# Optimization experiments

Measured on AMD Instinct MI355X. Metric: run time of the kernel, lower is better.

Reference implementation:

```python
import math
import jax, jax.numpy as jnp
import numpy as np
from math import factorial as fact

RS_IN = [(8, 0), (8, 1)]
RS_OUT = [(8, 0), (8, 1)]
N_PATH = 384
HIDDEN = 64
B, N_OUT_PTS, N_IN_PTS = 2, 256, 256

def _lfilters(l_in, l_out, lmax=10):
    return [l for l in range(abs(l_in - l_out), l_in + l_out + 1) if l <= lmax]

# ---- Clebsch-Gordan / Wigner-3j in the real spherical-harmonic basis ----
def _cg(j1, m1, j2, m2, j3, m3):
    if m1 + m2 != m3:
        return 0.0
    kmin = max(0, j2 - j3 - m1, j1 - j3 + m2)
    kmax = min(j1 + j2 - j3, j1 - m1, j2 + m2)
    if kmax < kmin:
        return 0.0
    pre = math.sqrt((2 * j3 + 1) * fact(j3 + j1 - j2) * fact(j3 - j1 + j2) * fact(j1 + j2 - j3) / fact(j1 + j2 + j3 + 1))
    pre *= math.sqrt(fact(j3 + m3) * fact(j3 - m3) * fact(j1 - m1) * fact(j1 + m1) * fact(j2 - m2) * fact(j2 + m2))
    s = sum((-1) ** k / (fact(k) * fact(j1 + j2 - j3 - k) * fact(j1 - m1 - k) * fact(j2 + m2 - k) * fact(j3 - j2 + m1 + k) * fact(j3 - j1 - m2 + k)) for k in range(kmin, kmax + 1))
    return pre * s

def _wigner3j(j1, j2, j3):
    W = np.zeros((2 * j1 + 1, 2 * j2 + 1, 2 * j3 + 1))
    for m1 in range(-j1, j1 + 1):
        for m2 in range(-j2, j2 + 1):
            m3 = -(m1 + m2)
            if abs(m3) <= j3:
                W[m1 + j1, m2 + j2, m3 + j3] = (-1) ** (j1 - j2 - m3) / math.sqrt(2 * j3 + 1) * _cg(j1, m1, j2, m2, j3, -m3)
    return W

def _A(l):
    # change of basis real<->complex SH: Y^real_a = sum_m A[a, m] Y^complex_m
    A = np.zeros((2 * l + 1, 2 * l + 1), dtype=np.complex128)
    A[l, l] = 1.0
    for m in range(1, l + 1):
        A[l + m, l + m] = (-1) ** m / math.sqrt(2)
        A[l + m, l - m] = 1.0 / math.sqrt(2)
        A[l - m, l - m] = 1j / math.sqrt(2)
        A[l - m, l + m] = -1j * (-1) ** m / math.sqrt(2)
    return A

def _real_cg(l1, l2, l3):
    W = _wigner3j(l1, l2, l3).astype(np.complex128)
    Q = np.einsum('am,bn,cp,mnp->abc', _A(l1).conj(), _A(l2).conj(), _A(l3).conj(), W)
    v = Q.flat[int(np.argmax(np.abs(Q)))]
    if abs(v) > 1e-12:
        Q = Q * (v.conjugate() / abs(v))  # rotate global phase so tensor is real
    assert np.abs(Q.imag).max() < 1e-8
    return Q.real.astype(np.float32)

# ---- real spherical harmonics of unit directions, l = 0, 1, 2 ----
_C0 = 0.28209479177387814
_C1 = 0.4886025119029199
_C2A = 1.0925484305920792
_C2B = 0.31539156525252005
_C2C = 0.5462742152960396

def _sh(xyz):
    r = jnp.linalg.norm(xyz, axis=-1, keepdims=True)
    u = xyz / jnp.maximum(r, 1e-12)
    x, y, z = u[..., 0], u[..., 1], u[..., 2]
    Y0 = _C0 * jnp.ones_like(x)[..., None]
    Y1 = _C1 * jnp.stack([y, z, x], axis=-1)
    Y2 = jnp.stack([_C2A * x * y, _C2A * y * z, _C2B * (3.0 * z * z - 1.0), _C2A * x * z, _C2C * (x * x - y * y)], axis=-1)
    return {0: Y0, 1: Y1, 2: Y2}


def setup_inputs() -> dict:
    key = jax.random.key(0)
    ks = jax.random.split(key, 3)
    dm = jax.random.normal(ks[0], (B, N_OUT_PTS, N_IN_PTS, 3), dtype=jnp.float32)
    W1 = 0.1 * jax.random.normal(ks[1], (1, HIDDEN), dtype=jnp.float32)
    b1 = jnp.zeros((HIDDEN,), dtype=jnp.float32)
    W2 = (1.0 / math.sqrt(HIDDEN)) * jax.random.normal(ks[2], (HIDDEN, N_PATH), dtype=jnp.float32)
    b2 = jnp.zeros((N_PATH,), dtype=jnp.float32)
    Q00 = jnp.asarray(_real_cg(0, 0, 0))  # (1,1,1)
    Q01 = jnp.asarray(_real_cg(0, 1, 1))  # (1,3,3)
    Q10 = jnp.asarray(_real_cg(1, 0, 1))  # (3,1,3)
    Q11 = jnp.asarray(np.concatenate([_real_cg(1, 1, l) for l in (0, 1, 2)], axis=2))  # (3,3,9)
    return {"difference_matrix": dm, "W1": W1, "b1": b1, "W2": W2, "b2": b2, "Q00": Q00, "Q01": Q01, "Q10": Q10, "Q11": Q11}


def reference(difference_matrix, W1, b1, W2, b2, Q00, Q01, Q10, Q11):
    Bb, No, Ni, _ = difference_matrix.shape
    Ys = _sh(difference_matrix)                       # l -> [B, No, Ni, 2l+1]
    radii = jnp.linalg.norm(difference_matrix, axis=-1)
    h = jax.nn.relu(radii[..., None] * W1[0] + b1)    # radial MLP
    weights = h @ W2 + b2                             # [B, No, Ni, N_PATH]
    Qs = {(0, 0): Q00, (0, 1): Q01, (1, 0): Q10, (1, 1): Q11}
    begin_w = 0
    rows = []
    for i, (mul_out, l_out) in enumerate(RS_OUT):
        num = sum(mul_in * len(_lfilters(l_in, l_out)) for mul_in, l_in in RS_IN) * Ni
        cols = []
        for j, (mul_in, l_in) in enumerate(RS_IN):
            lfs = _lfilters(l_in, l_out)
            n = mul_out * mul_in * len(lfs)
            w = weights[..., begin_w:begin_w + n].reshape(Bb, No, Ni, mul_out, mul_in, len(lfs))
            begin_w += n
            Q = Qs[(i, j)]
            K = 0.0
            off = 0
            for k, lf in enumerate(lfs):
                Qk = Q[:, :, off:off + 2 * lf + 1]
                off += 2 * lf + 1
                # i=m_out, j=m_in, r=m_filter, b n m = batch/N_out/N_in, u v = mul_out/mul_in
                K = K + jnp.einsum('ijr,bnmr,bnmuv->uivjbnm', Qk, Ys[lf], w[..., k])
            K = K * (math.sqrt(2 * l_in + 1) * math.sqrt(4.0 * math.pi) / math.sqrt(num))
            cols.append(K.reshape(mul_out * (2 * l_out + 1), mul_in * (2 * l_in + 1), Bb, No, Ni))
        rows.append(jnp.concatenate(cols, axis=1))
    return jnp.concatenate(rows, axis=0)  # [n_out, n_in, B, N_out, N_in]
```

## Files before the change

kernel.cpp:

```cpp
#include <hip/hip_runtime.h>
#include <math.h>

namespace {

typedef float f32x4 __attribute__((ext_vector_type(4)));
typedef float f32x2 __attribute__((ext_vector_type(2)));

constexpr int kPts  = 2 * 256 * 256;
constexpr int kHid  = 64;
constexpr int kPath = 384;

constexpr size_t kVOff    = (size_t)kPts * 4;
constexpr size_t kFlagOff = kVOff + kPath;
constexpr size_t kWOff    = kVOff + 512;
constexpr size_t kWFloats = 64ull * kPts * 6;
constexpr size_t kNeedBytes = (kWOff + kWFloats) * 4;

constexpr float kY0   = 0.28209479177387814f;
constexpr float kC1   = 0.4886025119029199f;
constexpr float kC2A  = 1.0925484305920792f;
constexpr float kC2B  = 0.31539156525252005f;
constexpr float kC2C  = 0.5462742152960396f;
constexpr float kS4pi = 3.5449077018110318f;
constexpr float kSq3  = 1.7320508075688772f;
constexpr float kN00  = kS4pi / 64.f;
constexpr float kN01  = kSq3 * kS4pi / 64.f;
constexpr float kN10  = kS4pi / 90.50966799187809f;
constexpr float kN11  = kSq3 * kS4pi / 90.50966799187809f;

__global__ __launch_bounds__(256)
void stage_kernel(const float* __restrict__ dm,
                  const float* __restrict__ W1,
                  const float* __restrict__ b1,
                  const float* __restrict__ W2,
                  f32x4* __restrict__ ru,
                  float* __restrict__ V,
                  unsigned* __restrict__ flag)
{
    const int pt = blockIdx.x * 256 + threadIdx.x;
    float dx = dm[3 * pt + 0], dy = dm[3 * pt + 1], dz = dm[3 * pt + 2];
    float r  = sqrtf(dx * dx + dy * dy + dz * dz);
    float inv = 1.0f / fmaxf(r, 1e-12f);
    f32x4 q; q.x = r; q.y = dx * inv; q.z = dy * inv; q.w = dz * inv;
    ru[pt] = q;

    if (blockIdx.x == 0) {
        for (int p = threadIdx.x; p < kPath; p += 256) {
            float acc = 0.f;
            for (int i = 0; i < kHid; ++i)
                acc += fmaxf(W1[i], 0.f) * W2[i * kPath + p];
            V[p] = acc;
        }
        if (threadIdx.x == 0) {
            unsigned f = 1u;
            for (int i = 0; i < kHid; ++i)
                if (b1[i] != 0.f) f = 0u;
            *flag = f;
        }
    }
}

__global__ __launch_bounds__(256)
void wstage_kernel(const float* __restrict__ W1,
                   const float* __restrict__ b1,
                   const float* __restrict__ W2,
                   const float* __restrict__ b2,
                   const f32x4* __restrict__ ru,
                   const unsigned* __restrict__ flag,
                   float* __restrict__ wout)
{
    if (*flag) return;
    const int pt = blockIdx.x * 256 + threadIdx.x;
    const float r = ru[pt].x;
    float h[kHid];
#pragma unroll
    for (int i = 0; i < kHid; ++i)
        h[i] = fmaxf(fmaf(r, W1[i], b1[i]), 0.f);

#pragma unroll 1
    for (int uv = 0; uv < 64; ++uv) {
        const int p[6] = { uv, 64 + uv, 128 + uv,
                           192 + 3 * uv, 193 + 3 * uv, 194 + 3 * uv };
        float acc[6];
#pragma unroll
        for (int c = 0; c < 6; ++c) acc[c] = b2[p[c]];
#pragma unroll 1
        for (int i = 0; i < kHid; ++i) {
            const float* row = W2 + (size_t)i * kPath;
#pragma unroll
            for (int c = 0; c < 6; ++c) acc[c] = fmaf(h[i], row[p[c]], acc[c]);
        }
        float* o = wout + ((size_t)uv * kPts + pt) * 6;
#pragma unroll
        for (int c = 0; c < 6; ++c) o[c] = acc[c];
    }
}

__global__ __launch_bounds__(256)
void sweep_kernel(const float* __restrict__ Q00,
                  const float* __restrict__ Q01,
                  const float* __restrict__ Q10,
                  const float* __restrict__ Q11,
                  const float* __restrict__ b2,
                  const f32x4* __restrict__ ru,
                  const float* __restrict__ V,
                  const unsigned* __restrict__ flag,
                  const float* __restrict__ wstaged,
                  float* __restrict__ out)
{
    const int seg = blockIdx.x;
    const int uv  = blockIdx.y;
    const int u = uv >> 3, v = uv & 7;

    const float s00p = kN00 * Q00[0] * kY0;
    float a01[3][3], a10[3][3], g0c[9], a11[9][3], b11[9][5];
    const float c2s[5] = { kC2A, kC2A, kC2B, kC2A, kC2C };
#pragma unroll
    for (int jc = 0; jc < 3; ++jc)
#pragma unroll
        for (int m = 0; m < 3; ++m)
            a01[jc][m] = kN01 * kC1 * Q01[jc * 3 + m];
#pragma unroll
    for (int ir = 0; ir < 3; ++ir)
#pragma unroll
        for (int m = 0; m < 3; ++m)
            a10[ir][m] = kN10 * kC1 * Q10[ir * 3 + m];
#pragma unroll
    for (int e = 0; e < 9; ++e) {
        g0c[e] = kN11 * kY0 * Q11[e * 9 + 0];
#pragma unroll
        for (int m = 0; m < 3; ++m) a11[e][m] = kN11 * kC1 * Q11[e * 9 + 1 + m];
#pragma unroll
        for (int m = 0; m < 5; ++m) b11[e][m] = kN11 * c2s[m] * Q11[e * 9 + 4 + m];
    }

    const bool fast = (*flag != 0u);
    const int pw[6] = { uv, 64 + uv, 128 + uv,
                        192 + 3 * uv, 193 + 3 * uv, 194 + 3 * uv };
    float vv[6], cc[6];
#pragma unroll
    for (int c = 0; c < 6; ++c) { vv[c] = V[pw[c]]; cc[c] = b2[pw[c]]; }

    int pr[16];
    pr[0] = u * 32 + v;
#pragma unroll
    for (int jc = 0; jc < 3; ++jc) pr[1 + jc] = u * 32 + 8 + v * 3 + jc;
#pragma unroll
    for (int ir = 0; ir < 3; ++ir) pr[4 + ir] = (8 + u * 3 + ir) * 32 + v;
#pragma unroll
    for (int e = 0; e < 9; ++e)
        pr[7 + e] = (8 + u * 3 + (e / 3)) * 32 + 8 + v * 3 + (e % 3);

    const size_t segbase = (size_t)seg * 4096 + threadIdx.x;

#pragma unroll 1
    for (int batch = 0; batch < 4; ++batch) {
        const size_t p0 = segbase + (size_t)batch * 1024;

        float bs[4][8], w_[4][6];
#pragma unroll
        for (int k = 0; k < 4; ++k) {
            f32x4 q = ru[p0 + k * 256];
            float r = q.x, x = q.y, y = q.z, z = q.w;
            bs[k][0] = y;  bs[k][1] = z;  bs[k][2] = x;
            bs[k][3] = x * y;
            bs[k][4] = y * z;
            bs[k][5] = fmaf(3.f * z, z, -1.f);
            bs[k][6] = x * z;
            bs[k][7] = fmaf(x, x, -(y * y));
            if (fast) {
#pragma unroll
                for (int c = 0; c < 6; ++c) w_[k][c] = fmaf(r, vv[c], cc[c]);
            } else {
                const float* wp = wstaged + ((size_t)uv * kPts + (p0 + k * 256)) * 6;
#pragma unroll
                for (int c = 0; c < 6; ++c) w_[k][c] = wp[c];
            }
        }

#pragma unroll
        for (int k = 0; k < 4; ++k)
            out[(size_t)pr[0] * kPts + p0 + k * 256] = s00p * w_[k][0];

#pragma unroll
        for (int jc = 0; jc < 3; ++jc) {
#pragma unroll
            for (int k = 0; k < 4; ++k) {
                float g = fmaf(a01[jc][2], bs[k][2],
                           fmaf(a01[jc][1], bs[k][1], a01[jc][0] * bs[k][0]));
                out[(size_t)pr[1 + jc] * kPts + p0 + k * 256] = g * w_[k][1];
            }
        }
#pragma unroll
        for (int ir = 0; ir < 3; ++ir) {
#pragma unroll
            for (int k = 0; k < 4; ++k) {
                float g = fmaf(a10[ir][2], bs[k][2],
                           fmaf(a10[ir][1], bs[k][1], a10[ir][0] * bs[k][0]));
                out[(size_t)pr[4 + ir] * kPts + p0 + k * 256] = g * w_[k][2];
            }
        }
#pragma unroll
        for (int e = 0; e < 9; ++e) {
#pragma unroll
            for (int k = 0; k < 4; ++k) {
                float lin = fmaf(a11[e][2], bs[k][2],
                             fmaf(a11[e][1], bs[k][1], a11[e][0] * bs[k][0]));
                float quad = b11[e][0] * bs[k][3];
#pragma unroll
                for (int m = 1; m < 5; ++m)
                    quad = fmaf(b11[e][m], bs[k][3 + m], quad);
                float val = fmaf(g0c[e], w_[k][3],
                             fmaf(lin, w_[k][4], quad * w_[k][5]));
                out[(size_t)pr[7 + e] * kPts + p0 + k * 256] = val;
            }
        }
    }
}

__global__ __launch_bounds__(256)
void mono_kernel(const float* __restrict__ dm,
                 const float* __restrict__ W1,
                 const float* __restrict__ b1,
                 const float* __restrict__ W2,
                 const float* __restrict__ b2,
                 const float* __restrict__ Q00,
                 const float* __restrict__ Q01,
                 const float* __restrict__ Q10,
                 const float* __restrict__ Q11,
                 float* __restrict__ out)
{
    const int g   = blockIdx.x * blockDim.x + threadIdx.x;
    const int uv0 = blockIdx.y * 8;

    const f32x4* dmv = reinterpret_cast<const f32x4*>(dm) + 3 * (size_t)g;
    f32x4 f0 = dmv[0], f1 = dmv[1], f2 = dmv[2];
    float px[4] = { f0.x, f0.w, f1.z, f2.y };
    float py[4] = { f0.y, f1.x, f1.w, f2.z };
    float pz[4] = { f0.z, f1.y, f2.x, f2.w };

    float r[4], ux[4], uy[4], uz[4];
#pragma unroll
    for (int p = 0; p < 4; ++p) {
        r[p] = sqrtf(px[p]*px[p] + py[p]*py[p] + pz[p]*pz[p]);
        float inv = 1.0f / fmaxf(r[p], 1e-12f);
        ux[p] = px[p]*inv; uy[p] = py[p]*inv; uz[p] = pz[p]*inv;
    }
    float Y10[4], Y11v[4], Y12[4], Y2[5][4];
#pragma unroll
    for (int p = 0; p < 4; ++p) {
        Y10[p] = kC1 * uy[p]; Y11v[p] = kC1 * uz[p]; Y12[p] = kC1 * ux[p];
        Y2[0][p] = kC2A * ux[p] * uy[p];
        Y2[1][p] = kC2A * uy[p] * uz[p];
        Y2[2][p] = kC2B * (3.f * uz[p] * uz[p] - 1.f);
        Y2[3][p] = kC2A * ux[p] * uz[p];
        Y2[4][p] = kC2C * (ux[p]*ux[p] - uy[p]*uy[p]);
    }
    const float s00 = kN00 * Q00[0] * kY0;
    float G0[9];
#pragma unroll
    for (int e = 0; e < 9; ++e) G0[e] = kN11 * Q11[e*9] * kY0;
    float g01[3][4], g10[3][4], G1[9][4], G2[9][4];
#pragma unroll
    for (int jc = 0; jc < 3; ++jc)
#pragma unroll
        for (int p = 0; p < 4; ++p)
            g01[jc][p] = kN01 * (Q01[jc*3]*Y10[p] + Q01[jc*3+1]*Y11v[p] + Q01[jc*3+2]*Y12[p]);
#pragma unroll
    for (int ir = 0; ir < 3; ++ir)
#pragma unroll
        for (int p = 0; p < 4; ++p)
            g10[ir][p] = kN10 * (Q10[ir*3]*Y10[p] + Q10[ir*3+1]*Y11v[p] + Q10[ir*3+2]*Y12[p]);
#pragma unroll
    for (int e = 0; e < 9; ++e) {
        const float* q = Q11 + e * 9;
#pragma unroll
        for (int p = 0; p < 4; ++p) {
            G1[e][p] = kN11 * (q[1]*Y10[p] + q[2]*Y11v[p] + q[3]*Y12[p]);
            G2[e][p] = kN11 * (q[4]*Y2[0][p] + q[5]*Y2[1][p] + q[6]*Y2[2][p] +
                               q[7]*Y2[3][p] + q[8]*Y2[4][p]);
        }
    }
    float* __restrict__ obase = out + 4 * (size_t)g;
    auto stf = [&](int row, const float* v4) {
        f32x4 q; q.x=v4[0]; q.y=v4[1]; q.z=v4[2]; q.w=v4[3];
        *reinterpret_cast<f32x4*>(obase + (size_t)row * kPts) = q;
    };
#pragma unroll 1
    for (int t = 0; t < 8; ++t) {
        const int uv = uv0 + t;
        float a00[4], a01v[4], a10v[4], a110[4], a111[4], a112[4];
#pragma unroll
        for (int p = 0; p < 4; ++p) {
            a00[p]=b2[uv]; a01v[p]=b2[64+uv]; a10v[p]=b2[128+uv];
            a110[p]=b2[192+3*uv]; a111[p]=b2[193+3*uv]; a112[p]=b2[194+3*uv];
        }
#pragma unroll 1
        for (int i = 0; i < kHid; ++i) {
            float w1i = W1[i], b1i = b1[i];
            const float* row = W2 + (size_t)i * kPath;
            float c00=row[uv], c01=row[64+uv], c10=row[128+uv];
            float c50=row[192+3*uv], c51=row[193+3*uv], c52=row[194+3*uv];
#pragma unroll
            for (int p = 0; p < 4; ++p) {
                float hi = fmaxf(fmaf(r[p], w1i, b1i), 0.f);
                a00[p]=fmaf(hi,c00,a00[p]); a01v[p]=fmaf(hi,c01,a01v[p]);
                a10v[p]=fmaf(hi,c10,a10v[p]); a110[p]=fmaf(hi,c50,a110[p]);
                a111[p]=fmaf(hi,c51,a111[p]); a112[p]=fmaf(hi,c52,a112[p]);
            }
        }
        const int u = uv >> 3, v = uv & 7;
        const int rowu = u * 32;
        float tmp[4];
#pragma unroll
        for (int p = 0; p < 4; ++p) tmp[p] = s00 * a00[p];
        stf(rowu + v, tmp);
#pragma unroll
        for (int jc = 0; jc < 3; ++jc) {
#pragma unroll
            for (int p = 0; p < 4; ++p) tmp[p] = g01[jc][p] * a01v[p];
            stf(rowu + 8 + v*3 + jc, tmp);
        }
#pragma unroll
        for (int ir = 0; ir < 3; ++ir) {
            const int rowb = (8 + u*3 + ir) * 32;
#pragma unroll
            for (int p = 0; p < 4; ++p) tmp[p] = g10[ir][p] * a10v[p];
            stf(rowb + v, tmp);
#pragma unroll
            for (int jc = 0; jc < 3; ++jc) {
                const int e = ir*3 + jc;
#pragma unroll
                for (int p = 0; p < 4; ++p)
                    tmp[p] = fmaf(G0[e], a110[p], fmaf(G1[e][p], a111[p], G2[e][p]*a112[p]));
                stf(rowb + 8 + v*3 + jc, tmp);
            }
        }
    }
}

}

extern "C" void kernel_launch(void* const* d_in, const int* in_sizes, int n_in,
                              void* d_out, int out_size, void* d_ws, size_t ws_size,
                              hipStream_t stream)
{
    const float* dm  = (const float*)d_in[0];
    const float* W1  = (const float*)d_in[1];
    const float* b1  = (const float*)d_in[2];
    const float* W2  = (const float*)d_in[3];
    const float* b2  = (const float*)d_in[4];
    const float* Q00 = (const float*)d_in[5];
    const float* Q01 = (const float*)d_in[6];
    const float* Q10 = (const float*)d_in[7];
    const float* Q11 = (const float*)d_in[8];
    float* out = (float*)d_out;

    if (ws_size >= kNeedBytes) {
        float* ws = (float*)d_ws;
        f32x4*    ru   = (f32x4*)ws;
        float*    V    = ws + kVOff;
        unsigned* flag = (unsigned*)(ws + kFlagOff);
        float*    wst  = ws + kWOff;
        stage_kernel<<<kPts / 256, 256, 0, stream>>>(dm, W1, b1, W2, ru, V, flag);
        wstage_kernel<<<kPts / 256, 256, 0, stream>>>(W1, b1, W2, b2, ru, flag, wst);
        sweep_kernel<<<dim3(32, 64), 256, 0, stream>>>(
            Q00, Q01, Q10, Q11, b2, ru, V, flag, wst, out);
    } else {
        mono_kernel<<<dim3(128, 8), 256, 0, stream>>>(
            dm, W1, b1, W2, b2, Q00, Q01, Q10, Q11, out);
    }
}
```

Measured before the change: 113.9 us.

## Fuse direction computation into a single plane-writing kernel with per-thread point tiling

Replaces the three-kernel pipeline (stage directions, stage per-point weights, sweep) with a tiny prep kernel for V and the bias flag, plus one fused kernel. The fused kernel recomputes the norm and unit direction from the raw displacements in each (u,v) block, and computes the radial MLP inline on the slow path. Each thread now handles 8 points instead of 4. This removes the intermediate workspace traffic and launches, at the cost of redundant sqrt/divide work and repeated displacement reads across the 64 uv blocks.

```diff
diff --git a/kernel.cpp b/kernel.cpp
--- a/kernel.cpp
+++ b/kernel.cpp
@@ -4,17 +4,12 @@
 namespace {
 
 typedef float f32x4 __attribute__((ext_vector_type(4)));
-typedef float f32x2 __attribute__((ext_vector_type(2)));
 
 constexpr int kPts  = 2 * 256 * 256;
 constexpr int kHid  = 64;
 constexpr int kPath = 384;
 
-constexpr size_t kVOff    = (size_t)kPts * 4;
-constexpr size_t kFlagOff = kVOff + kPath;
-constexpr size_t kWOff    = kVOff + 512;
-constexpr size_t kWFloats = 64ull * kPts * 6;
-constexpr size_t kNeedBytes = (kWOff + kWFloats) * 4;
+constexpr size_t kWsNeedBytes = (kPath + 1) * sizeof(float);
 
 constexpr float kY0   = 0.28209479177387814f;
 constexpr float kC1   = 0.4886025119029199f;
@@ -28,192 +23,142 @@
 constexpr float kN10  = kS4pi / 90.50966799187809f;
 constexpr float kN11  = kSq3 * kS4pi / 90.50966799187809f;
 
+__global__ void prep_kernel(const float* __restrict__ W1,
+                            const float* __restrict__ b1,
+                            const float* __restrict__ W2,
+                            float* __restrict__ V,
+                            unsigned* __restrict__ flag)
+{
+    int t = blockIdx.x * 256 + threadIdx.x;
+    if (t < kPath) {
+        float acc = 0.f;
+        for (int i = 0; i < kHid; ++i)
+            acc += fmaxf(W1[i], 0.f) * W2[i * kPath + t];
+        V[t] = acc;
+    }
+    if (t == 0) {
+        unsigned f = 1u;
+        for (int i = 0; i < kHid; ++i)
+            if (b1[i] != 0.f) f = 0u;
+        *flag = f;
+    }
+}
+
 __global__ __launch_bounds__(256)
-void stage_kernel(const float* __restrict__ dm,
+void plane_kernel(const float* __restrict__ dm,
                   const float* __restrict__ W1,
                   const float* __restrict__ b1,
                   const float* __restrict__ W2,
-                  f32x4* __restrict__ ru,
-                  float* __restrict__ V,
-                  unsigned* __restrict__ flag)
-{
-    const int pt = blockIdx.x * 256 + threadIdx.x;
-    float dx = dm[3 * pt + 0], dy = dm[3 * pt + 1], dz = dm[3 * pt + 2];
-    float r  = sqrtf(dx * dx + dy * dy + dz * dz);
-    float inv = 1.0f / fmaxf(r, 1e-12f);
-    f32x4 q; q.x = r; q.y = dx * inv; q.z = dy * inv; q.w = dz * inv;
-    ru[pt] = q;
-
-    if (blockIdx.x == 0) {
-        for (int p = threadIdx.x; p < kPath; p += 256) {
-            float acc = 0.f;
-            for (int i = 0; i < kHid; ++i)
-                acc += fmaxf(W1[i], 0.f) * W2[i * kPath + p];
-            V[p] = acc;
-        }
-        if (threadIdx.x == 0) {
-            unsigned f = 1u;
-            for (int i = 0; i < kHid; ++i)
-                if (b1[i] != 0.f) f = 0u;
-            *flag = f;
-        }
-    }
-}
-
-__global__ __launch_bounds__(256)
-void wstage_kernel(const float* __restrict__ W1,
-                   const float* __restrict__ b1,
-                   const float* __restrict__ W2,
-                   const float* __restrict__ b2,
-                   const f32x4* __restrict__ ru,
-                   const unsigned* __restrict__ flag,
-                   float* __restrict__ wout)
-{
-    if (*flag) return;
-    const int pt = blockIdx.x * 256 + threadIdx.x;
-    const float r = ru[pt].x;
-    float h[kHid];
-#pragma unroll
-    for (int i = 0; i < kHid; ++i)
-        h[i] = fmaxf(fmaf(r, W1[i], b1[i]), 0.f);
-
-#pragma unroll 1
-    for (int uv = 0; uv < 64; ++uv) {
-        const int p[6] = { uv, 64 + uv, 128 + uv,
-                           192 + 3 * uv, 193 + 3 * uv, 194 + 3 * uv };
-        float acc[6];
-#pragma unroll
-        for (int c = 0; c < 6; ++c) acc[c] = b2[p[c]];
-#pragma unroll 1
-        for (int i = 0; i < kHid; ++i) {
-            const float* row = W2 + (size_t)i * kPath;
-#pragma unroll
-            for (int c = 0; c < 6; ++c) acc[c] = fmaf(h[i], row[p[c]], acc[c]);
-        }
-        float* o = wout + ((size_t)uv * kPts + pt) * 6;
-#pragma unroll
-        for (int c = 0; c < 6; ++c) o[c] = acc[c];
-    }
-}
-
-__global__ __launch_bounds__(256)
-void sweep_kernel(const float* __restrict__ Q00,
+                  const float* __restrict__ b2,
+                  const float* __restrict__ Q00,
                   const float* __restrict__ Q01,
                   const float* __restrict__ Q10,
                   const float* __restrict__ Q11,
-                  const float* __restrict__ b2,
-                  const f32x4* __restrict__ ru,
                   const float* __restrict__ V,
                   const unsigned* __restrict__ flag,
-                  const float* __restrict__ wstaged,
                   float* __restrict__ out)
 {
-    const int seg = blockIdx.x;
-    const int uv  = blockIdx.y;
-    const int u = uv >> 3, v = uv & 7;
-
-    const float s00p = kN00 * Q00[0] * kY0;
-    float a01[3][3], a10[3][3], g0c[9], a11[9][3], b11[9][5];
-    const float c2s[5] = { kC2A, kC2A, kC2B, kC2A, kC2C };
-#pragma unroll
-    for (int jc = 0; jc < 3; ++jc)
-#pragma unroll
-        for (int m = 0; m < 3; ++m)
-            a01[jc][m] = kN01 * kC1 * Q01[jc * 3 + m];
-#pragma unroll
-    for (int ir = 0; ir < 3; ++ir)
-#pragma unroll
-        for (int m = 0; m < 3; ++m)
-            a10[ir][m] = kN10 * kC1 * Q10[ir * 3 + m];
-#pragma unroll
-    for (int e = 0; e < 9; ++e) {
-        g0c[e] = kN11 * kY0 * Q11[e * 9 + 0];
-#pragma unroll
-        for (int m = 0; m < 3; ++m) a11[e][m] = kN11 * kC1 * Q11[e * 9 + 1 + m];
-#pragma unroll
-        for (int m = 0; m < 5; ++m) b11[e][m] = kN11 * c2s[m] * Q11[e * 9 + 4 + m];
-    }
-
-    const bool fast = (*flag != 0u);
+    const int uv = blockIdx.y, u = uv >> 3, v = uv & 7;
+    const size_t base = (size_t)blockIdx.x * 2048 + threadIdx.x;
+
+    float R[8], X[8], Y[8], Z[8];
+#pragma unroll
+    for (int k = 0; k < 8; ++k) {
+        size_t pt = base + 256 * (size_t)k;
+        float dx = dm[3 * pt], dy = dm[3 * pt + 1], dz = dm[3 * pt + 2];
+        float r  = sqrtf(dx * dx + dy * dy + dz * dz);
+        float inv = 1.f / fmaxf(r, 1e-12f);
+        R[k] = r; X[k] = dx * inv; Y[k] = dy * inv; Z[k] = dz * inv;
+    }
+
     const int pw[6] = { uv, 64 + uv, 128 + uv,
                         192 + 3 * uv, 193 + 3 * uv, 194 + 3 * uv };
-    float vv[6], cc[6];
-#pragma unroll
-    for (int c = 0; c < 6; ++c) { vv[c] = V[pw[c]]; cc[c] = b2[pw[c]]; }
-
-    int pr[16];
-    pr[0] = u * 32 + v;
-#pragma unroll
-    for (int jc = 0; jc < 3; ++jc) pr[1 + jc] = u * 32 + 8 + v * 3 + jc;
-#pragma unroll
-    for (int ir = 0; ir < 3; ++ir) pr[4 + ir] = (8 + u * 3 + ir) * 32 + v;
-#pragma unroll
-    for (int e = 0; e < 9; ++e)
-        pr[7 + e] = (8 + u * 3 + (e / 3)) * 32 + 8 + v * 3 + (e % 3);
-
-    const size_t segbase = (size_t)seg * 4096 + threadIdx.x;
-
-#pragma unroll 1
-    for (int batch = 0; batch < 4; ++batch) {
-        const size_t p0 = segbase + (size_t)batch * 1024;
-
-        float bs[4][8], w_[4][6];
-#pragma unroll
-        for (int k = 0; k < 4; ++k) {
-            f32x4 q = ru[p0 + k * 256];
-            float r = q.x, x = q.y, y = q.z, z = q.w;
-            bs[k][0] = y;  bs[k][1] = z;  bs[k][2] = x;
-            bs[k][3] = x * y;
-            bs[k][4] = y * z;
-            bs[k][5] = fmaf(3.f * z, z, -1.f);
-            bs[k][6] = x * z;
-            bs[k][7] = fmaf(x, x, -(y * y));
-            if (fast) {
-#pragma unroll
-                for (int c = 0; c < 6; ++c) w_[k][c] = fmaf(r, vv[c], cc[c]);
-            } else {
-                const float* wp = wstaged + ((size_t)uv * kPts + (p0 + k * 256)) * 6;
-#pragma unroll
-                for (int c = 0; c < 6; ++c) w_[k][c] = wp[c];
+    float w[6][8];
+    if (*flag != 0u) {
+#pragma unroll
+        for (int c = 0; c < 6; ++c) {
+            float vc = V[pw[c]], bc = b2[pw[c]];
+#pragma unroll
+            for (int k = 0; k < 8; ++k) w[c][k] = fmaf(R[k], vc, bc);
+        }
+    } else {
+#pragma unroll
+        for (int c = 0; c < 6; ++c) {
+            float bc = b2[pw[c]];
+#pragma unroll
+            for (int k = 0; k < 8; ++k) w[c][k] = bc;
+        }
+#pragma unroll 1
+        for (int i = 0; i < kHid; ++i) {
+            float w1i = W1[i], b1i = b1[i];
+            const float* row = W2 + (size_t)i * kPath;
+            float cr[6];
+#pragma unroll
+            for (int c = 0; c < 6; ++c) cr[c] = row[pw[c]];
+#pragma unroll
+            for (int k = 0; k < 8; ++k) {
+                float h = fmaxf(fmaf(R[k], w1i, b1i), 0.f);
+#pragma unroll
+                for (int c = 0; c < 6; ++c) w[c][k] = fmaf(h, cr[c], w[c][k]);
             }
         }
-
-#pragma unroll
-        for (int k = 0; k < 4; ++k)
-            out[(size_t)pr[0] * kPts + p0 + k * 256] = s00p * w_[k][0];
-
-#pragma unroll
-        for (int jc = 0; jc < 3; ++jc) {
-#pragma unroll
-            for (int k = 0; k < 4; ++k) {
-                float g = fmaf(a01[jc][2], bs[k][2],
-                           fmaf(a01[jc][1], bs[k][1], a01[jc][0] * bs[k][0]));
-                out[(size_t)pr[1 + jc] * kPts + p0 + k * 256] = g * w_[k][1];
-            }
-        }
-#pragma unroll
-        for (int ir = 0; ir < 3; ++ir) {
-#pragma unroll
-            for (int k = 0; k < 4; ++k) {
-                float g = fmaf(a10[ir][2], bs[k][2],
-                           fmaf(a10[ir][1], bs[k][1], a10[ir][0] * bs[k][0]));
-                out[(size_t)pr[4 + ir] * kPts + p0 + k * 256] = g * w_[k][2];
-            }
-        }
-#pragma unroll
-        for (int e = 0; e < 9; ++e) {
-#pragma unroll
-            for (int k = 0; k < 4; ++k) {
-                float lin = fmaf(a11[e][2], bs[k][2],
-                             fmaf(a11[e][1], bs[k][1], a11[e][0] * bs[k][0]));
-                float quad = b11[e][0] * bs[k][3];
-#pragma unroll
-                for (int m = 1; m < 5; ++m)
-                    quad = fmaf(b11[e][m], bs[k][3 + m], quad);
-                float val = fmaf(g0c[e], w_[k][3],
-                             fmaf(lin, w_[k][4], quad * w_[k][5]));
-                out[(size_t)pr[7 + e] * kPts + p0 + k * 256] = val;
-            }
+    }
+
+    float* __restrict__ oseg = out + base;
+
+    {
+        float s00p = kN00 * Q00[0] * kY0;
+        float* o = oseg + (size_t)(u * 32 + v) * kPts;
+#pragma unroll
+        for (int k = 0; k < 8; ++k) o[256 * k] = s00p * w[0][k];
+    }
+#pragma unroll 1
+    for (int jc = 0; jc < 3; ++jc) {
+        float a0 = kN01 * kC1 * Q01[jc * 3 + 0];
+        float a1 = kN01 * kC1 * Q01[jc * 3 + 1];
+        float a2 = kN01 * kC1 * Q01[jc * 3 + 2];
+        float* o = oseg + (size_t)(u * 32 + 8 + v * 3 + jc) * kPts;
+#pragma unroll
+        for (int k = 0; k < 8; ++k) {
+            float g = fmaf(a2, X[k], fmaf(a1, Z[k], a0 * Y[k]));
+            o[256 * k] = g * w[1][k];
+        }
+    }
+#pragma unroll 1
+    for (int ir = 0; ir < 3; ++ir) {
+        float a0 = kN10 * kC1 * Q10[ir * 3 + 0];
+        float a1 = kN10 * kC1 * Q10[ir * 3 + 1];
+        float a2 = kN10 * kC1 * Q10[ir * 3 + 2];
+        float* o = oseg + (size_t)((8 + u * 3 + ir) * 32 + v) * kPts;
+#pragma unroll
+        for (int k = 0; k < 8; ++k) {
+            float g = fmaf(a2, X[k], fmaf(a1, Z[k], a0 * Y[k]));
+            o[256 * k] = g * w[2][k];
+        }
+    }
+#pragma unroll 1
+    for (int e = 0; e < 9; ++e) {
+        const float* q = Q11 + e * 9;
+        float g0 = kN11 * kY0 * q[0];
+        float a0 = kN11 * kC1 * q[1];
+        float a1 = kN11 * kC1 * q[2];
+        float a2 = kN11 * kC1 * q[3];
+        float b0 = kN11 * kC2A * q[4];
+        float b1c = kN11 * kC2A * q[5];
+        float b2c = kN11 * kC2B * q[6];
+        float b3 = kN11 * kC2A * q[7];
+        float b4 = kN11 * kC2C * q[8];
+        float* o = oseg + (size_t)((8 + u * 3 + e / 3) * 32 + 8 + v * 3 + e % 3) * kPts;
+#pragma unroll
+        for (int k = 0; k < 8; ++k) {
+            float lin = fmaf(a2, X[k], fmaf(a1, Z[k], a0 * Y[k]));
+            float zz  = fmaf(3.f * Z[k], Z[k], -1.f);
+            float quad = fmaf(b0, X[k] * Y[k],
+                         fmaf(b1c, Y[k] * Z[k],
+                         fmaf(b2c, zz,
+                         fmaf(b3, X[k] * Z[k],
+                              b4 * fmaf(X[k], X[k], -(Y[k] * Y[k]))))));
+            o[256 * k] = fmaf(g0, w[3][k], fmaf(lin, w[4][k], quad * w[5][k]));
         }
     }
 }
@@ -356,18 +301,14 @@
     const float* Q11 = (const float*)d_in[8];
     float* out = (float*)d_out;
 
-    if (ws_size >= kNeedBytes) {
-        float* ws = (float*)d_ws;
-        f32x4*    ru   = (f32x4*)ws;
-        float*    V    = ws + kVOff;
-        unsigned* flag = (unsigned*)(ws + kFlagOff);
-        float*    wst  = ws + kWOff;
-        stage_kernel<<<kPts / 256, 256, 0, stream>>>(dm, W1, b1, W2, ru, V, flag);
-        wstage_kernel<<<kPts / 256, 256, 0, stream>>>(W1, b1, W2, b2, ru, flag, wst);
-        sweep_kernel<<<dim3(32, 64), 256, 0, stream>>>(
-            Q00, Q01, Q10, Q11, b2, ru, V, flag, wst, out);
+    if (ws_size >= kWsNeedBytes) {
+        float*    V    = (float*)d_ws;
+        unsigned* flag = (unsigned*)(V + kPath);
+        prep_kernel<<<2, 256, 0, stream>>>(W1, b1, W2, V, flag);
+        plane_kernel<<<dim3(kPts / 2048, 64), 256, 0, stream>>>(
+            dm, W1, b1, W2, b2, Q00, Q01, Q10, Q11, V, flag, out);
     } else {
-        mono_kernel<<<dim3(128, 8), 256, 0, stream>>>(
+        mono_kernel<<<dim3(kPts / 4 / 256, 8), 256, 0, stream>>>(
             dm, W1, b1, W2, b2, Q00, Q01, Q10, Q11, out);
     }
 }
```

Measured after the change: 112.0 us. Within noise of the previous version (-1.7%).
